# Kernel optimization log

Hardware: AMD Instinct MI355X
Metric: run time of the kernel (lower is better)

The kernel has to match this reference:

```python
import jax, jax.numpy as jnp
import numpy as np

NUM_REL = 7
EPS = 1e-5
N, E = 30000, 480000
D_IN, D_H = 21, 512


def _bn(x, g, b):
    # BatchNorm1d over nodes (training-mode batch statistics, biased var like torch)
    mu = x.mean(axis=0)
    var = x.var(axis=0)
    return (x - mu) * jax.lax.rsqrt(var + EPS) * g + b


def _conv(x, src, seg_idx, lin_w, lin_b, self_w, self_b, bn_g, bn_b):
    # GeometricRelationalGraphConv: gather src features, scatter-add per (dst, relation)
    d = x.shape[1]
    msg = x[src]                                                   # (E, d)
    upd = jax.ops.segment_sum(msg, seg_idx, num_segments=N * NUM_REL)
    upd = upd.reshape(N, NUM_REL * d)                              # (N, 7*d)
    out = upd @ lin_w.T + lin_b + x @ self_w.T + self_b            # linear + self-loop
    out = _bn(out, bn_g, bn_b)                                     # conv-internal BN
    return jax.nn.relu(out)


def setup_inputs() -> dict:
    key = jax.random.key(0)
    ks = jax.random.split(key, 16)
    inp = {
        "x": jax.random.normal(ks[0], (N, D_IN), dtype=jnp.float32),
        "src": jax.random.randint(ks[1], (E,), 0, N, dtype=jnp.int32),
        "dst": jax.random.randint(ks[2], (E,), 0, N, dtype=jnp.int32),
        "rel": jax.random.randint(ks[3], (E,), 0, NUM_REL, dtype=jnp.int32),
    }
    dims = [(D_IN, D_H), (D_H, D_H), (D_H, D_H)]
    k = 4
    for i, (din, dout) in enumerate(dims):
        inp[f"lin_w{i}"] = jax.random.normal(ks[k], (dout, NUM_REL * din), dtype=jnp.float32) * 0.05
        inp[f"self_w{i}"] = jax.random.normal(ks[k + 1], (dout, din), dtype=jnp.float32) * 0.05
        k += 2
        inp[f"lin_b{i}"] = jnp.zeros((dout,), jnp.float32)
        inp[f"self_b{i}"] = jnp.zeros((dout,), jnp.float32)
        inp[f"bn1_g{i}"] = jnp.ones((dout,), jnp.float32)
        inp[f"bn1_b{i}"] = jnp.zeros((dout,), jnp.float32)
        inp[f"bn2_g{i}"] = jnp.ones((dout,), jnp.float32)
        inp[f"bn2_b{i}"] = jnp.zeros((dout,), jnp.float32)
    return inp


def reference(x, src, dst, rel,
              lin_w0, lin_b0, self_w0, self_b0, bn1_g0, bn1_b0, bn2_g0, bn2_b0,
              lin_w1, lin_b1, self_w1, self_b1, bn1_g1, bn1_b1, bn2_g1, bn2_b1,
              lin_w2, lin_b2, self_w2, self_b2, bn1_g2, bn1_b2, bn2_g2, bn2_b2):
    seg_idx = dst * NUM_REL + rel                                  # (E,)
    layers = [
        (lin_w0, lin_b0, self_w0, self_b0, bn1_g0, bn1_b0, bn2_g0, bn2_b0),
        (lin_w1, lin_b1, self_w1, self_b1, bn1_g1, bn1_b1, bn2_g1, bn2_b1),
        (lin_w2, lin_b2, self_w2, self_b2, bn1_g2, bn1_b2, bn2_g2, bn2_b2),
    ]
    hiddens = []
    h = x
    for lw, lb, sw, sb, g1, b1, g2, b2 in layers:
        h = _conv(h, src, seg_idx, lw, lb, sw, sb, g1, b1)
        h = _bn(h, g2, b2)                                         # GearNet outer BN
        hiddens.append(h)
    return jnp.concatenate(hiddens, axis=-1)                      # (N, 3*512) concat_hidden
```

## Files before the change

kernel.cpp:

```cpp
#include <hip/hip_runtime.h>

#define NN   30000
#define NE   480000
#define NR   7
#define NSEG (NN*NR)
#define DH   512
#define DIN  21
#define EPSB 1e-5f
#define KSEG 3584

typedef __attribute__((ext_vector_type(8))) short bf16x8;
typedef __attribute__((ext_vector_type(8))) unsigned short u16x8;
typedef __attribute__((ext_vector_type(4))) float f32x4;
typedef unsigned short ushortT;

static inline size_t align256(size_t x){ return (x + 255) & ~(size_t)255; }

__device__ inline float bf2f(ushortT u){
    unsigned int i = ((unsigned int)u) << 16; float f; __builtin_memcpy(&f, &i, 4); return f;
}
__device__ inline ushortT f2bf(float f){
    unsigned int i; __builtin_memcpy(&i, &f, 4);
    unsigned int r = i + 0x7FFFu + ((i >> 16) & 1u);
    return (ushortT)(r >> 16);
}

__device__ inline void load_lds16(const ushortT* g, ushortT* l){
    __builtin_amdgcn_global_load_lds((const __attribute__((address_space(1))) unsigned int*)g,
                                     (__attribute__((address_space(3))) unsigned int*)l,
                                     16, 0, 0);
}


__global__ void hist_k(const int* __restrict__ dst, const int* __restrict__ rel,
                       int* __restrict__ counts){
    int e = blockIdx.x*256 + threadIdx.x;
    if (e < NE) atomicAdd(&counts[dst[e]*NR + rel[e]], 1);
}

__global__ void scan1_k(const int* __restrict__ counts, int* __restrict__ bsum){
    __shared__ int sd[256];
    int t = threadIdx.x;
    int base = blockIdx.x*1024 + t*4;
    int s = 0;
#pragma unroll
    for (int i = 0; i < 4; i++){ int idx = base + i; if (idx < NSEG) s += counts[idx]; }
    sd[t] = s; __syncthreads();
    for (int off = 128; off > 0; off >>= 1){
        if (t < off) sd[t] += sd[t+off];
        __syncthreads();
    }
    if (t == 0) bsum[blockIdx.x] = sd[0];
}

__global__ void scan2_k(int* __restrict__ bsum, int nb, int* __restrict__ seg_start){
    __shared__ int sd[256];
    int t = threadIdx.x;
    int v = (t < nb) ? bsum[t] : 0;
    sd[t] = v; __syncthreads();
    for (int off = 1; off < 256; off <<= 1){
        int x = sd[t];
        if (t >= off) x += sd[t-off];
        __syncthreads();
        sd[t] = x; __syncthreads();
    }
    if (t < nb) bsum[t] = (t == 0) ? 0 : sd[t-1];
    if (t == 0) seg_start[NSEG] = NE;
}

__global__ void scan3_k(const int* __restrict__ counts, const int* __restrict__ bsum,
                        int* __restrict__ seg_start){
    __shared__ int sd[256];
    int t = threadIdx.x;
    int base = blockIdx.x*1024 + t*4;
    int v[4]; int s = 0;
#pragma unroll
    for (int i = 0; i < 4; i++){ int idx = base + i; v[i] = (idx < NSEG) ? counts[idx] : 0; s += v[i]; }
    sd[t] = s; __syncthreads();
    for (int off = 1; off < 256; off <<= 1){
        int x = sd[t];
        if (t >= off) x += sd[t-off];
        __syncthreads();
        sd[t] = x; __syncthreads();
    }
    int excl = sd[t] - s + bsum[blockIdx.x];
#pragma unroll
    for (int i = 0; i < 4; i++){
        int idx = base + i;
        if (idx < NSEG){ seg_start[idx] = excl; excl += v[i]; }
    }
}

__global__ void scatter_k(const int* __restrict__ src, const int* __restrict__ dst,
                          const int* __restrict__ rel, const int* __restrict__ seg_start,
                          int* __restrict__ cursor, int* __restrict__ src_sorted){
    int e = blockIdx.x*256 + threadIdx.x;
    if (e < NE){
        int s = dst[e]*NR + rel[e];
        int pos = seg_start[s] + atomicAdd(&cursor[s], 1);
        src_sorted[pos] = src[e];
    }
}


__global__ void segsum21b_k(const float* __restrict__ x0,
                            const int* __restrict__ seg_start, const int* __restrict__ src_sorted,
                            ushortT* __restrict__ Acat0){
    int n = blockIdx.x;
    int t = threadIdx.x;
    ushortT* arow = Acat0 + (long)n*256;
    if (t < DIN){
        int sb = n*NR;
        int e0 = seg_start[sb];
#pragma unroll
        for (int r = 0; r < NR; r++){
            int e1 = seg_start[sb + r + 1];
            float a = 0.f;
            for (int e = e0; e < e1; e++) a += x0[(long)src_sorted[e]*DIN + t];
            e0 = e1;
            arow[r*DIN + t] = f2bf(a);
        }
        arow[7*DIN + t] = f2bf(x0[(long)n*DIN + t]);
    }
    if (t >= 40) arow[168 + (t - 40)] = 0;
    arow[192 + t] = 0;
}


__device__ inline void segsum_body(const ushortT* __restrict__ hbf,
                                   const int* __restrict__ seg_start,
                                   const int* __restrict__ src_sorted,
                                   ushortT* __restrict__ Acat,
                                   int wid, int c0, int lane){
    const int n = c0 + wid;
    const int co = lane*8;

    int sb[8];
#pragma unroll
    for (int i = 0; i < 8; i++) sb[i] = seg_start[n*NR + i];

    ushortT* arow = Acat + (long)wid*KSEG + co;
#pragma unroll
    for (int r = 0; r < NR; r++){
        float a[8];
#pragma unroll
        for (int j = 0; j < 8; j++) a[j] = 0.f;
        int e = sb[r], e1 = sb[r+1];
        for (; e + 3 < e1; e += 4){
            u16x8 v0 = *reinterpret_cast<const u16x8*>(hbf + (long)src_sorted[e  ]*DH + co);
            u16x8 v1 = *reinterpret_cast<const u16x8*>(hbf + (long)src_sorted[e+1]*DH + co);
            u16x8 v2 = *reinterpret_cast<const u16x8*>(hbf + (long)src_sorted[e+2]*DH + co);
            u16x8 v3 = *reinterpret_cast<const u16x8*>(hbf + (long)src_sorted[e+3]*DH + co);
#pragma unroll
            for (int j = 0; j < 8; j++)
                a[j] += (bf2f((ushortT)v0[j]) + bf2f((ushortT)v1[j]))
                      + (bf2f((ushortT)v2[j]) + bf2f((ushortT)v3[j]));
        }
        for (; e < e1; e++){
            u16x8 v = *reinterpret_cast<const u16x8*>(hbf + (long)src_sorted[e]*DH + co);
#pragma unroll
            for (int j = 0; j < 8; j++) a[j] += bf2f((ushortT)v[j]);
        }
        u16x8 o;
#pragma unroll
        for (int j = 0; j < 8; j++) o[j] = f2bf(a[j]);
        *reinterpret_cast<u16x8*>(arow + r*DH) = o;
    }
}

__global__ __launch_bounds__(256)
void segsum_wave_k(const ushortT* __restrict__ hbf,
                   const int* __restrict__ seg_start, const int* __restrict__ src_sorted,
                   ushortT* __restrict__ Acat, int c0, int cn){
    const int lane = threadIdx.x & 63;
    const int gwave = (blockIdx.x*256 + threadIdx.x) >> 6;
    const int nwaves = (gridDim.x*256) >> 6;
    for (int wid = gwave; wid < cn; wid += nwaves)
        segsum_body(hbf, seg_start, src_sorted, Acat, wid, c0, lane);
}


__global__ void convw_k(const float* __restrict__ lw, const float* __restrict__ sw,
                        int d, int Kp, ushortT* __restrict__ Wc){
    int i = blockIdx.x*256 + threadIdx.x;
    if (i < DH*Kp){
        int n = i / Kp, k = i % Kp;
        float v;
        if (k < 7*d)      v = lw[(long)n*7*d + k];
        else if (k < 8*d) v = sw[(long)n*d + (k - 7*d)];
        else              v = 0.f;
        Wc[i] = f2bf(v);
    }
}


__global__ __launch_bounds__(512, 2)
void gemm8_k(const ushortT* __restrict__ A, int lda, int ntA,
             const ushortT* __restrict__ hbase, int M,
             const ushortT* __restrict__ W, int ldw,
             const float* __restrict__ b1, const float* __restrict__ b2,
             float* __restrict__ C, int ldc, int nt, float* __restrict__ sums){
    __shared__ ushortT As[2*2*128*64];
    __shared__ ushortT Bs[2*2*128*64];
    const int t = threadIdx.x;

    const int nwg = gridDim.x;
    int qq = nwg >> 3, rr = nwg & 7;
    int xcd = blockIdx.x & 7, slot = blockIdx.x >> 3;
    int l = xcd*qq + min(xcd, rr) + slot;
    const int bm = (l >> 1)*256;
    const int bn = (l & 1)*256;

    const int ur0 = t >> 3, ur1 = (t + 512) >> 3;
    const int sw0 = ((t & 7) ^ (ur0 & 7))*8;
    const int sw1 = ((t & 7) ^ (ur1 & 7))*8;
    const int a00 = min(bm + ur0, M-1),       a01 = min(bm + ur1, M-1);
    const int a10 = min(bm + 128 + ur0, M-1), a11 = min(bm + 128 + ur1, M-1);
    const int b00 = bn + ur0,       b01 = bn + ur1;
    const int b10 = bn + 128 + ur0, b11 = bn + 128 + ur1;

    auto stageA = [&](int kt, int h, int buf){
        ushortT* d = &As[(buf*2 + h)*8192];
        int r0 = h ? a10 : a00, r1 = h ? a11 : a01;
        const ushortT* p0;
        const ushortT* p1;
        if (kt < ntA){
            p0 = A + (long)r0*lda + kt*64 + sw0;
            p1 = A + (long)r1*lda + kt*64 + sw1;
        } else {
            int k0 = (kt - ntA)*64;
            p0 = hbase + (long)r0*DH + k0 + sw0;
            p1 = hbase + (long)r1*DH + k0 + sw1;
        }
        load_lds16(p0, d + t*8);
        load_lds16(p1, d + (t + 512)*8);
    };
    auto stageB = [&](int kt, int h, int buf){
        ushortT* d = &Bs[(buf*2 + h)*8192];
        int r0 = h ? b10 : b00, r1 = h ? b11 : b01;
        load_lds16(W + (long)r0*ldw + kt*64 + sw0, d + t*8);
        load_lds16(W + (long)r1*ldw + kt*64 + sw1, d + (t + 512)*8);
    };

    const int w = t >> 6, lane = t & 63;
    const int wm = w >> 2, wn = w & 3;
    const int r = lane & 15, hi = lane >> 4;
    const int swzk0 = ((hi)     ^ (r & 7))*8;
    const int swzk1 = ((4 + hi) ^ (r & 7))*8;
    const int aBase = wm*8192 + r*64;
    const int bBase = (wn >> 1)*8192 + ((wn & 1)*64 + r)*64;

    f32x4 acc[8][4];
#pragma unroll
    for (int m = 0; m < 8; m++)
#pragma unroll
        for (int n = 0; n < 4; n++) acc[m][n] = (f32x4){0.f,0.f,0.f,0.f};

    stageA(0, 0, 0); stageA(0, 1, 0);
    stageB(0, 0, 0); stageB(0, 1, 0);
    stageA(1, 0, 1); stageA(1, 1, 1);
    asm volatile("s_waitcnt vmcnt(4)" ::: "memory");
    __builtin_amdgcn_s_barrier();

    for (int it = 0; it < nt; it += 2){
#pragma unroll
        for (int b = 0; b < 2; ++b){
            bf16x8 aK0[8], aK1[8];
            const int bufo = b*16384;
#pragma unroll
            for (int qp = 0; qp < 4; ++qp){
                const int np = qp >> 1;
                const int swzk = (qp & 1) ? swzk1 : swzk0;
                bf16x8 bb0 = *reinterpret_cast<const bf16x8*>(&Bs[bufo + bBase + (np*2+0)*1024 + swzk]);
                bf16x8 bb1 = *reinterpret_cast<const bf16x8*>(&Bs[bufo + bBase + (np*2+1)*1024 + swzk]);
                if (qp == 0){
#pragma unroll
                    for (int m = 0; m < 8; m++)
                        aK0[m] = *reinterpret_cast<const bf16x8*>(&As[bufo + aBase + m*1024 + swzk0]);
                }
                if (qp == 1){
#pragma unroll
                    for (int m = 0; m < 8; m++)
                        aK1[m] = *reinterpret_cast<const bf16x8*>(&As[bufo + aBase + m*1024 + swzk1]);
                }
                {
                    const int ph = b*4 + qp;
                    if (ph == 0)      stageB(min(it+1, nt-1), 0, 1);
                    else if (ph == 1) stageB(min(it+1, nt-1), 1, 1);
                    else if (ph == 2) stageA(min(it+2, nt-1), 0, 0);
                    else if (ph == 3) stageA(min(it+2, nt-1), 1, 0);
                    else if (ph == 4) stageB(min(it+2, nt-1), 0, 0);
                    else if (ph == 5) stageB(min(it+2, nt-1), 1, 0);
                    else if (ph == 6) stageA(min(it+3, nt-1), 0, 1);
                    else              stageA(min(it+3, nt-1), 1, 1);
                }
                __builtin_amdgcn_s_barrier();
                asm volatile("s_waitcnt lgkmcnt(0)" ::: "memory");
                __builtin_amdgcn_sched_barrier(0);
                __builtin_amdgcn_s_setprio(1);
#pragma unroll
                for (int m = 0; m < 8; m++){
                    const bf16x8 am = (qp & 1) ? aK1[m] : aK0[m];
                    acc[m][np*2+0] = __builtin_amdgcn_mfma_f32_16x16x32_bf16(am, bb0, acc[m][np*2+0], 0, 0, 0);
                    acc[m][np*2+1] = __builtin_amdgcn_mfma_f32_16x16x32_bf16(am, bb1, acc[m][np*2+1], 0, 0, 0);
                }
                __builtin_amdgcn_s_setprio(0);
                if (qp == 3) asm volatile("s_waitcnt vmcnt(2)" ::: "memory");
                __builtin_amdgcn_s_barrier();
            }
        }
    }
    asm volatile("s_waitcnt vmcnt(0)" ::: "memory");

#pragma unroll
    for (int n = 0; n < 4; n++){
        int col = bn + wn*64 + n*16 + r;
        float bb = b1[col] + b2[col];
        float s = 0.f, s2 = 0.f;
#pragma unroll
        for (int m = 0; m < 8; m++){
            int row = bm + wm*128 + m*16 + hi*4;
#pragma unroll
            for (int j2 = 0; j2 < 4; j2++){
                if (row + j2 < M){
                    float v = acc[m][n][j2] + bb;
                    C[(long)(row + j2)*ldc + col] = v;
                    s += v; s2 = fmaf(v, v, s2);
                }
            }
        }
        s  += __shfl_xor(s, 16);  s  += __shfl_xor(s, 32);
        s2 += __shfl_xor(s2, 16); s2 += __shfl_xor(s2, 32);
        if (hi == 0){
            atomicAdd(&sums[col], s);
            atomicAdd(&sums[DH + col], s2);
        }
    }
}


__global__ void finalize_k(const float* __restrict__ sums, const float* __restrict__ g,
                           const float* __restrict__ b, float* __restrict__ ac){
    int c = blockIdx.x*256 + threadIdx.x;
    if (c < DH){
        float mu  = sums[c] * (1.f/NN);
        float var = sums[DH + c] * (1.f/NN) - mu*mu;
        var = fmaxf(var, 0.f);
        float a = g[c] * rsqrtf(var + EPSB);
        ac[c]      = a;
        ac[DH + c] = fmaf(-mu, a, b[c]);
    }
}

__global__ void bnrelu_k(float* __restrict__ o, int M, const float* __restrict__ ac,
                         float* __restrict__ sums2){
    int col = blockIdx.x*256 + threadIdx.x;
    int r0 = blockIdx.y*128;
    int r1 = min(r0 + 128, M);
    float a = ac[col], c = ac[DH + col];
    float s = 0.f, s2 = 0.f;
    for (int r = r0; r < r1; r++){
        long idx = (long)r*(3*DH) + col;
        float y = fmaxf(fmaf(a, o[idx], c), 0.f);
        o[idx] = y;
        s += y; s2 = fmaf(y, y, s2);
    }
    atomicAdd(&sums2[col], s);
    atomicAdd(&sums2[DH + col], s2);
}

__global__ void bn2write_k(float* __restrict__ o, const float* __restrict__ ac,
                           ushortT* __restrict__ hbf){
    long i = (long)blockIdx.x*256 + threadIdx.x;
    if (i < (long)NN*DH){
        int r = (int)(i >> 9);
        int c = (int)(i & 511);
        long idx = (long)r*(3*DH) + c;
        float h = fmaf(ac[c], o[idx], ac[DH + c]);
        o[idx] = h;
        hbf[i] = f2bf(h);
    }
}


extern "C" void kernel_launch(void* const* d_in, const int* in_sizes, int n_in,
                              void* d_out, int out_size, void* d_ws, size_t ws_size,
                              hipStream_t stream){
    const float* x0  = (const float*)d_in[0];
    const int*   src = (const int*)d_in[1];
    const int*   dst = (const int*)d_in[2];
    const int*   rel = (const int*)d_in[3];
    const float* lin_w[3]  = {(const float*)d_in[4],  (const float*)d_in[12], (const float*)d_in[20]};
    const float* self_w[3] = {(const float*)d_in[5],  (const float*)d_in[13], (const float*)d_in[21]};
    const float* lin_b[3]  = {(const float*)d_in[6],  (const float*)d_in[14], (const float*)d_in[22]};
    const float* self_b[3] = {(const float*)d_in[7],  (const float*)d_in[15], (const float*)d_in[23]};
    const float* bn1_g[3]  = {(const float*)d_in[8],  (const float*)d_in[16], (const float*)d_in[24]};
    const float* bn1_b[3]  = {(const float*)d_in[9],  (const float*)d_in[17], (const float*)d_in[25]};
    const float* bn2_g[3]  = {(const float*)d_in[10], (const float*)d_in[18], (const float*)d_in[26]};
    const float* bn2_b[3]  = {(const float*)d_in[11], (const float*)d_in[19], (const float*)d_in[27]};

    char* ws = (char*)d_ws;
    size_t off = 0;
    auto alloc = [&](size_t bytes)->char*{ char* p = ws + off; off = align256(off + bytes); return p; };

    int*     seg_start  = (int*)alloc((size_t)(NSEG+1)*4);
    int*     bsum       = (int*)alloc(1024*4);
    int*     src_sorted = (int*)alloc((size_t)NE*4);
    float*   stats      = (float*)alloc((size_t)8*DH*4);
    float*   sums1 = stats;            float* sums2 = stats + 2*DH;
    float*   ac1   = stats + 4*DH;     float* ac2   = stats + 6*DH;
    ushortT* hbf    = (ushortT*)alloc((size_t)NN*DH*2);
    ushortT* Wcat   = (ushortT*)alloc((size_t)DH*4096*2);

    size_t remain = (ws_size > off) ? (ws_size - off) : 0;
    ushortT* Acat   = (ushortT*)(ws + off);
    int*     counts = (int*)Acat;
    int*     cursor = counts + NSEG;
    ushortT* Acat0  = (ushortT*)align256((size_t)(cursor + NSEG));

    long max_nodes = (long)(remain / ((size_t)KSEG*2));
    int chunk;
    if (max_nodes >= NN) chunk = NN;
    else { chunk = (int)(max_nodes & ~255L); if (chunk < 2560) chunk = 2560; }

    hipMemsetAsync(counts, 0, (size_t)NSEG*4, stream);
    hipMemsetAsync(cursor, 0, (size_t)NSEG*4, stream);
    hist_k<<<(NE+255)/256, 256, 0, stream>>>(dst, rel, counts);
    int nb = (NSEG + 1023)/1024;
    scan1_k<<<nb, 256, 0, stream>>>(counts, bsum);
    scan2_k<<<1, 256, 0, stream>>>(bsum, nb, seg_start);
    scan3_k<<<nb, 256, 0, stream>>>(counts, bsum, seg_start);
    scatter_k<<<(NE+255)/256, 256, 0, stream>>>(src, dst, rel, seg_start, cursor, src_sorted);

    float* dout = (float*)d_out;

    for (int layer = 0; layer < 3; layer++){
        int d  = (layer == 0) ? DIN : DH;
        int Kp = (layer == 0) ? 256 : 4096;
        convw_k<<<(DH*Kp + 255)/256, 256, 0, stream>>>(lin_w[layer], self_w[layer], d, Kp, Wcat);
        hipMemsetAsync(stats, 0, (size_t)4*DH*4, stream);

        if (layer == 0){
            segsum21b_k<<<NN, 64, 0, stream>>>(x0, seg_start, src_sorted, Acat0);
            gemm8_k<<<((NN + 255)/256)*2, 512, 0, stream>>>(
                Acat0, 256, 4, Acat0, NN, Wcat, 256,
                lin_b[layer], self_b[layer],
                dout + layer*DH, 3*DH, 4, sums1);
        } else {
            for (int c0 = 0; c0 < NN; c0 += chunk){
                int cn = (NN - c0 < chunk) ? (NN - c0) : chunk;
                int sgrid = (cn + 3)/4; if (sgrid > 2048) sgrid = 2048;
                segsum_wave_k<<<sgrid, 256, 0, stream>>>(
                    hbf, seg_start, src_sorted, Acat, c0, cn);
                gemm8_k<<<((cn + 255)/256)*2, 512, 0, stream>>>(
                    Acat, KSEG, 56, hbf + (long)c0*DH, cn, Wcat, 4096,
                    lin_b[layer], self_b[layer],
                    dout + (long)c0*(3*DH) + layer*DH, 3*DH, 64, sums1);
            }
        }

        finalize_k<<<2, 256, 0, stream>>>(sums1, bn1_g[layer], bn1_b[layer], ac1);
        bnrelu_k<<<dim3(2, (NN+127)/128), 256, 0, stream>>>(dout + layer*DH, NN, ac1, sums2);
        finalize_k<<<2, 256, 0, stream>>>(sums2, bn2_g[layer], bn2_b[layer], ac2);
        bn2write_k<<<((long)NN*DH + 255)/256, 256, 0, stream>>>(dout + layer*DH, ac2, hbf);
    }
}
```

Measured before the change: 948.7 us.

## Simplify GEMM to single-stage double buffering and fuse BN-relu write into final pass

The GEMM main loop drops the deep two-stage prefetch schedule with per-phase barriers. It now uses a plain double buffer: load the current tile's fragments, issue the next tile's global loads, run the MFMAs, and take one barrier per iteration. The launch-bounds occupancy hint is removed. The BN1+ReLU pass becomes a read-only statistics kernel, and the final write pass recomputes ReLU(BN1) before BN2, which removes one full write of the output slab. The bf16 hidden copy is skipped on the last layer. The simpler pipeline may hide global-load latency less well than the previous multi-stage schedule.

Result: faster. 865.4 us (-8.8%).

```diff
diff --git a/kernel.cpp b/kernel.cpp
--- a/kernel.cpp
+++ b/kernel.cpp
@@ -194,8 +194,8 @@
 }
 
 
-__global__ __launch_bounds__(512, 2)
-void gemm8_k(const ushortT* __restrict__ A, int lda, int ntA,
+__global__ __launch_bounds__(512)
+void gemmX_k(const ushortT* __restrict__ A, int lda, int ntA,
              const ushortT* __restrict__ hbase, int M,
              const ushortT* __restrict__ W, int ldw,
              const float* __restrict__ b1, const float* __restrict__ b2,
@@ -258,59 +258,54 @@
 
     stageA(0, 0, 0); stageA(0, 1, 0);
     stageB(0, 0, 0); stageB(0, 1, 0);
-    stageA(1, 0, 1); stageA(1, 1, 1);
-    asm volatile("s_waitcnt vmcnt(4)" ::: "memory");
+    asm volatile("s_waitcnt vmcnt(0)" ::: "memory");
     __builtin_amdgcn_s_barrier();
 
-    for (int it = 0; it < nt; it += 2){
-#pragma unroll
-        for (int b = 0; b < 2; ++b){
-            bf16x8 aK0[8], aK1[8];
-            const int bufo = b*16384;
-#pragma unroll
-            for (int qp = 0; qp < 4; ++qp){
-                const int np = qp >> 1;
-                const int swzk = (qp & 1) ? swzk1 : swzk0;
-                bf16x8 bb0 = *reinterpret_cast<const bf16x8*>(&Bs[bufo + bBase + (np*2+0)*1024 + swzk]);
-                bf16x8 bb1 = *reinterpret_cast<const bf16x8*>(&Bs[bufo + bBase + (np*2+1)*1024 + swzk]);
-                if (qp == 0){
-#pragma unroll
-                    for (int m = 0; m < 8; m++)
-                        aK0[m] = *reinterpret_cast<const bf16x8*>(&As[bufo + aBase + m*1024 + swzk0]);
-                }
-                if (qp == 1){
-#pragma unroll
-                    for (int m = 0; m < 8; m++)
-                        aK1[m] = *reinterpret_cast<const bf16x8*>(&As[bufo + aBase + m*1024 + swzk1]);
-                }
-                {
-                    const int ph = b*4 + qp;
-                    if (ph == 0)      stageB(min(it+1, nt-1), 0, 1);
-                    else if (ph == 1) stageB(min(it+1, nt-1), 1, 1);
-                    else if (ph == 2) stageA(min(it+2, nt-1), 0, 0);
-                    else if (ph == 3) stageA(min(it+2, nt-1), 1, 0);
-                    else if (ph == 4) stageB(min(it+2, nt-1), 0, 0);
-                    else if (ph == 5) stageB(min(it+2, nt-1), 1, 0);
-                    else if (ph == 6) stageA(min(it+3, nt-1), 0, 1);
-                    else              stageA(min(it+3, nt-1), 1, 1);
-                }
-                __builtin_amdgcn_s_barrier();
-                asm volatile("s_waitcnt lgkmcnt(0)" ::: "memory");
-                __builtin_amdgcn_sched_barrier(0);
-                __builtin_amdgcn_s_setprio(1);
-#pragma unroll
-                for (int m = 0; m < 8; m++){
-                    const bf16x8 am = (qp & 1) ? aK1[m] : aK0[m];
-                    acc[m][np*2+0] = __builtin_amdgcn_mfma_f32_16x16x32_bf16(am, bb0, acc[m][np*2+0], 0, 0, 0);
-                    acc[m][np*2+1] = __builtin_amdgcn_mfma_f32_16x16x32_bf16(am, bb1, acc[m][np*2+1], 0, 0, 0);
-                }
-                __builtin_amdgcn_s_setprio(0);
-                if (qp == 3) asm volatile("s_waitcnt vmcnt(2)" ::: "memory");
-                __builtin_amdgcn_s_barrier();
-            }
-        }
-    }
-    asm volatile("s_waitcnt vmcnt(0)" ::: "memory");
+    for (int j = 0; j < nt; ++j){
+        const int buf = j & 1;
+        const int aoff = buf*16384;
+        const int boff = buf*16384;
+        const bool haveNext = (j + 1 < nt);
+
+        bf16x8 aK[8], bK[4];
+#pragma unroll
+        for (int m = 0; m < 8; m++)
+            aK[m] = *reinterpret_cast<const bf16x8*>(&As[aoff + aBase + m*1024 + swzk0]);
+#pragma unroll
+        for (int n = 0; n < 4; n++)
+            bK[n] = *reinterpret_cast<const bf16x8*>(&Bs[boff + bBase + n*1024 + swzk0]);
+        if (haveNext){
+            stageA(j + 1, 0, buf ^ 1); stageA(j + 1, 1, buf ^ 1);
+            stageB(j + 1, 0, buf ^ 1); stageB(j + 1, 1, buf ^ 1);
+        }
+        asm volatile("s_waitcnt lgkmcnt(0)" ::: "memory");
+        __builtin_amdgcn_sched_barrier(0);
+        __builtin_amdgcn_s_setprio(1);
+#pragma unroll
+        for (int m = 0; m < 8; m++)
+#pragma unroll
+            for (int n = 0; n < 4; n++)
+                acc[m][n] = __builtin_amdgcn_mfma_f32_16x16x32_bf16(aK[m], bK[n], acc[m][n], 0, 0, 0);
+        __builtin_amdgcn_s_setprio(0);
+#pragma unroll
+        for (int m = 0; m < 8; m++)
+            aK[m] = *reinterpret_cast<const bf16x8*>(&As[aoff + aBase + m*1024 + swzk1]);
+#pragma unroll
+        for (int n = 0; n < 4; n++)
+            bK[n] = *reinterpret_cast<const bf16x8*>(&Bs[boff + bBase + n*1024 + swzk1]);
+        asm volatile("s_waitcnt lgkmcnt(0)" ::: "memory");
+        __builtin_amdgcn_sched_barrier(0);
+        __builtin_amdgcn_s_setprio(1);
+#pragma unroll
+        for (int m = 0; m < 8; m++)
+#pragma unroll
+            for (int n = 0; n < 4; n++)
+                acc[m][n] = __builtin_amdgcn_mfma_f32_16x16x32_bf16(aK[m], bK[n], acc[m][n], 0, 0, 0);
+        __builtin_amdgcn_s_setprio(0);
+
+        asm volatile("s_waitcnt vmcnt(0)" ::: "memory");
+        __builtin_amdgcn_s_barrier();
+    }
 
 #pragma unroll
     for (int n = 0; n < 4; n++){
@@ -352,33 +347,33 @@
     }
 }
 
-__global__ void bnrelu_k(float* __restrict__ o, int M, const float* __restrict__ ac,
-                         float* __restrict__ sums2){
+__global__ void brstats_k(const float* __restrict__ o, int M, const float* __restrict__ ac,
+                          float* __restrict__ sums2){
     int col = blockIdx.x*256 + threadIdx.x;
     int r0 = blockIdx.y*128;
     int r1 = min(r0 + 128, M);
     float a = ac[col], c = ac[DH + col];
     float s = 0.f, s2 = 0.f;
     for (int r = r0; r < r1; r++){
-        long idx = (long)r*(3*DH) + col;
-        float y = fmaxf(fmaf(a, o[idx], c), 0.f);
-        o[idx] = y;
+        float y = fmaxf(fmaf(a, o[(long)r*(3*DH) + col], c), 0.f);
         s += y; s2 = fmaf(y, y, s2);
     }
     atomicAdd(&sums2[col], s);
     atomicAdd(&sums2[DH + col], s2);
 }
 
-__global__ void bn2write_k(float* __restrict__ o, const float* __restrict__ ac,
-                           ushortT* __restrict__ hbf){
+__global__ void bn2write_k(float* __restrict__ o, const float* __restrict__ ac1,
+                           const float* __restrict__ ac2, ushortT* __restrict__ hbf,
+                           int writeH){
     long i = (long)blockIdx.x*256 + threadIdx.x;
     if (i < (long)NN*DH){
         int r = (int)(i >> 9);
         int c = (int)(i & 511);
         long idx = (long)r*(3*DH) + c;
-        float h = fmaf(ac[c], o[idx], ac[DH + c]);
+        float y = fmaxf(fmaf(ac1[c], o[idx], ac1[DH + c]), 0.f);
+        float h = fmaf(ac2[c], y, ac2[DH + c]);
         o[idx] = h;
-        hbf[i] = f2bf(h);
+        if (writeH) hbf[i] = f2bf(h);
     }
 }
 
@@ -442,7 +437,7 @@
 
         if (layer == 0){
             segsum21b_k<<<NN, 64, 0, stream>>>(x0, seg_start, src_sorted, Acat0);
-            gemm8_k<<<((NN + 255)/256)*2, 512, 0, stream>>>(
+            gemmX_k<<<((NN + 255)/256)*2, 512, 0, stream>>>(
                 Acat0, 256, 4, Acat0, NN, Wcat, 256,
                 lin_b[layer], self_b[layer],
                 dout + layer*DH, 3*DH, 4, sums1);
@@ -452,7 +447,7 @@
                 int sgrid = (cn + 3)/4; if (sgrid > 2048) sgrid = 2048;
                 segsum_wave_k<<<sgrid, 256, 0, stream>>>(
                     hbf, seg_start, src_sorted, Acat, c0, cn);
-                gemm8_k<<<((cn + 255)/256)*2, 512, 0, stream>>>(
+                gemmX_k<<<((cn + 255)/256)*2, 512, 0, stream>>>(
                     Acat, KSEG, 56, hbf + (long)c0*DH, cn, Wcat, 4096,
                     lin_b[layer], self_b[layer],
                     dout + (long)c0*(3*DH) + layer*DH, 3*DH, 64, sums1);
@@ -460,8 +455,9 @@
         }
 
         finalize_k<<<2, 256, 0, stream>>>(sums1, bn1_g[layer], bn1_b[layer], ac1);
-        bnrelu_k<<<dim3(2, (NN+127)/128), 256, 0, stream>>>(dout + layer*DH, NN, ac1, sums2);
+        brstats_k<<<dim3(2, (NN+127)/128), 256, 0, stream>>>(dout + layer*DH, NN, ac1, sums2);
         finalize_k<<<2, 256, 0, stream>>>(sums2, bn2_g[layer], bn2_b[layer], ac2);
-        bn2write_k<<<((long)NN*DH + 255)/256, 256, 0, stream>>>(dout + layer*DH, ac2, hbf);
-    }
-}
+        bn2write_k<<<((long)NN*DH + 255)/256, 256, 0, stream>>>(
+            dout + layer*DH, ac1, ac2, hbf, (layer < 2) ? 1 : 0);
+    }
+}
```
